# Kernel optimization log

Hardware: AMD Instinct MI355X
Metric: run time of the kernel (lower is better)

The kernel has to match this reference:

```python
import jax, jax.numpy as jnp
import numpy as np

B, T, C, H = 128, 256, 384, 6
D = C // H  # head dim = 64


def setup_inputs() -> dict:
    key = jax.random.key(0)
    k1, k2, k3, k4, k5 = jax.random.split(key, 5)
    s = 0.02
    return {
        "x": jax.random.normal(k1, (B, T, C), dtype=jnp.float32),
        "W_qkv": jax.random.normal(k2, (C, 3 * C), dtype=jnp.float32) * s,
        "b_qkv": jax.random.normal(k3, (3 * C,), dtype=jnp.float32) * s,
        "W_proj": jax.random.normal(k4, (C, C), dtype=jnp.float32) * s,
        "b_proj": jax.random.normal(k5, (C,), dtype=jnp.float32) * s,
    }


def reference(x, W_qkv, b_qkv, W_proj, b_proj):
    Bv, Tv, Cv = x.shape
    # fused QKV projection, then split
    qkv = x @ W_qkv + b_qkv                      # [B,T,3C]
    q, k, v = jnp.split(qkv, 3, axis=-1)
    # [B,T,C] -> [B,H,T,D]
    q = q.reshape(Bv, Tv, H, D).transpose(0, 2, 1, 3)
    k = k.reshape(Bv, Tv, H, D).transpose(0, 2, 1, 3)
    v = v.reshape(Bv, Tv, H, D).transpose(0, 2, 1, 3)
    # causal masked scores, scaled by head_dim**-0.5
    scores = jnp.einsum("bhqd,bhkd->bhqk", q, k) * (D ** -0.5)
    causal = jnp.tril(jnp.ones((Tv, Tv), dtype=bool))
    scores = jnp.where(causal, scores, -jnp.inf)
    wt = jax.nn.softmax(scores, axis=-1)
    # dropout layers are identity in eval mode
    out = jnp.einsum("bhqk,bhkd->bhqd", wt, v)   # [B,H,T,D]
    out = out.transpose(0, 2, 1, 3).reshape(Bv, Tv, Cv)
    return out @ W_proj + b_proj
```

## Files before the change

### kernel.cpp

```cpp
#include <hip/hip_runtime.h>

typedef unsigned short u16;
typedef unsigned int u32;
typedef __attribute__((ext_vector_type(4))) float f32x4;
typedef __attribute__((ext_vector_type(8))) __bf16 bf16x8;
typedef __attribute__((ext_vector_type(2))) __bf16 bf16x2;

#define NEGINF (-1e30f)
#define QSCALE 0.18033688011112042f

__device__ __forceinline__ u16 f32_to_bf16(float f) {
  union { float f; unsigned int u; } v;
  v.f = f;
  unsigned int u = v.u;
  u += 0x7fffu + ((u >> 16) & 1u);
  return (u16)(u >> 16);
}

__device__ __forceinline__ u32 pk_bf16(float a, float b) {
  bf16x2 t;
  t.x = (__bf16)a;
  t.y = (__bf16)b;
  return __builtin_bit_cast(u32, t);
}

__device__ __forceinline__ f32x4 mfma_bf16(bf16x8 a, bf16x8 b, f32x4 c) {
  return __builtin_amdgcn_mfma_f32_16x16x32_bf16(a, b, c, 0, 0, 0);
}

#define GLOAD_LDS16(g, l) __builtin_amdgcn_global_load_lds( \
    (const __attribute__((address_space(1))) unsigned int*)(g), \
    (__attribute__((address_space(3))) unsigned int*)(l), 16, 0, 0)

__global__ void k_cvt_all(const float4* __restrict__ x4, u16* __restrict__ xb,
                          const float* __restrict__ Wqkv, u16* __restrict__ wqkvb,
                          const float* __restrict__ Wproj, u16* __restrict__ wprojb) {
  const int bidx = (int)blockIdx.x;
  if (bidx < 12288) {
    int i = bidx * 256 + threadIdx.x;
    float4 v = x4[i];
    uint2 o;
    o.x = (unsigned int)f32_to_bf16(v.x) | ((unsigned int)f32_to_bf16(v.y) << 16);
    o.y = (unsigned int)f32_to_bf16(v.z) | ((unsigned int)f32_to_bf16(v.w) << 16);
    *(uint2*)(xb + (size_t)i * 4) = o;
  } else if (bidx < 14016) {
    int idx = (bidx - 12288) * 256 + threadIdx.x;
    if (idx < 384 * 1152) {
      int k = idx / 1152, n = idx - k * 1152;
      wqkvb[(size_t)n * 384 + k] = f32_to_bf16(Wqkv[idx]);
    }
  } else {
    int idx = (bidx - 14016) * 256 + threadIdx.x;
    if (idx < 384 * 384) {
      int k = idx / 384, n = idx - k * 384;
      wprojb[(size_t)n * 384 + k] = f32_to_bf16(Wproj[idx]);
    }
  }
}

template <bool SW>
__device__ __forceinline__ void gemm256x64(
    const u16* __restrict__ A, const u16* __restrict__ Bt,
    int mBase, int nBase, u16* lsA, u16* lsB,
    f32x4 acc[4][2], int lane, int wv, int wm, int wn) {
  const int l15 = lane & 15;
  size_t aoff[4];
  u32 aldso[4];
#pragma unroll
  for (int jj = 0; jj < 4; ++jj) {
    int c = wv * 256 + jj * 64 + lane;
    int row = c >> 3;
    int kc = (c & 7) ^ (row & 7);
    aoff[jj] = (size_t)(mBase + row) * 384 + kc * 8;
    aldso[jj] = (u32)(wv * 256 + jj * 64) * 8;
  }
  int cb = wv * 64 + lane;
  int brow = cb >> 3;
  size_t boff = (size_t)(nBase + brow) * 384 + (size_t)(((cb & 7) ^ (brow & 7)) * 8);
  u32 bldso = (u32)(wv * 64) * 8;

#define STAGE_T(kt, buf) do { \
  _Pragma("unroll") \
  for (int jj = 0; jj < 4; ++jj) \
    GLOAD_LDS16(A + aoff[jj] + (kt), lsA + (buf) * 16384 + aldso[jj]); \
  GLOAD_LDS16(Bt + boff + (kt), lsB + (buf) * 4096 + bldso); \
  } while (0)

  STAGE_T(0, 0);
#pragma unroll
  for (int t = 0; t < 6; ++t) {
    const int cur = t & 1;
    if (t < 5) {
      STAGE_T((t + 1) * 64, cur ^ 1);
      asm volatile("s_waitcnt vmcnt(5)" ::: "memory");
    } else {
      asm volatile("s_waitcnt vmcnt(0)" ::: "memory");
    }
    __builtin_amdgcn_s_barrier();
    const char* bA = (const char*)(lsA + cur * 16384);
    const char* bB = (const char*)(lsB + cur * 4096);
#pragma unroll
    for (int ks = 0; ks < 2; ++ks) {
      bf16x8 af[4], bfr[2];
#pragma unroll
      for (int i = 0; i < 4; ++i) {
        int row = wm * 64 + i * 16 + l15;
        af[i] = *(const bf16x8*)(bA + row * 128 + (((ks * 4 + (lane >> 4)) ^ (row & 7)) << 4));
      }
#pragma unroll
      for (int j = 0; j < 2; ++j) {
        int row = wn * 32 + j * 16 + l15;
        bfr[j] = *(const bf16x8*)(bB + row * 128 + (((ks * 4 + (lane >> 4)) ^ (row & 7)) << 4));
      }
#pragma unroll
      for (int i = 0; i < 4; ++i)
#pragma unroll
        for (int j = 0; j < 2; ++j)
          acc[i][j] = SW ? mfma_bf16(bfr[j], af[i], acc[i][j])
                         : mfma_bf16(af[i], bfr[j], acc[i][j]);
    }
    __builtin_amdgcn_s_barrier();
  }
#undef STAGE_T
}

__global__ __launch_bounds__(512, 4) void k_qkv(
    const u16* __restrict__ A, const u16* __restrict__ Bt,
    const float* __restrict__ bias,
    u16* __restrict__ Qb, u16* __restrict__ Kb, u16* __restrict__ Vtb) {
  __shared__ __align__(16) u16 lsA[2 * 16384];
  __shared__ __align__(16) u16 lsB[2 * 4096];
  const int tid = threadIdx.x, lane = tid & 63, wv = tid >> 6;
  const int l15 = lane & 15, g = lane >> 4;
  const int wm = wv >> 1, wn = wv & 1;
  const int bid = (int)blockIdx.x;
  const int wgid = (bid & 7) * 288 + (bid >> 3);
  const int mtile = wgid / 18, ntile = wgid % 18;
  const int mBase = mtile * 256, nBase = ntile * 64;
  const int part = ntile / 6;
  const int hh = ntile % 6;
  char* ot = (char*)lsA;

  f32x4 acc[4][2] = {};
  if (part == 2) {
    gemm256x64<false>(A, Bt, mBase, nBase, lsA, lsB, acc, lane, wv, wm, wn);
#pragma unroll
    for (int j = 0; j < 2; ++j) {
      int drow = wn * 32 + j * 16 + l15;
      float bv = bias[nBase + drow];
#pragma unroll
      for (int i = 0; i < 4; ++i) {
        int t0 = wm * 64 + i * 16 + g * 4;
        uint2 w;
        w.x = pk_bf16(acc[i][j][0] + bv, acc[i][j][1] + bv);
        w.y = pk_bf16(acc[i][j][2] + bv, acc[i][j][3] + bv);
        int byte = (drow * 512 + t0 * 2) ^ ((drow & 7) << 4);
        *(uint2*)(ot + byte) = w;
      }
    }
    asm volatile("s_waitcnt lgkmcnt(0)" ::: "memory");
    __builtin_amdgcn_s_barrier();
    size_t obase = (size_t)(mtile * 6 + hh) * (64 * 256);
#pragma unroll
    for (int p = 0; p < 4; ++p) {
      int idx = p * 512 + tid;
      int row = idx >> 5, c = idx & 31;
      uint4 v = *(const uint4*)(ot + row * 512 + (((c ^ (row & 7)) << 4)));
      *(uint4*)(Vtb + obase + (size_t)row * 256 + c * 8) = v;
    }
  } else {
    gemm256x64<true>(A, Bt, mBase, nBase, lsA, lsB, acc, lane, wv, wm, wn);
    const float scale = (part == 0) ? QSCALE : 1.0f;
    u16* dst = (part == 0) ? Qb : Kb;
#pragma unroll
    for (int j = 0; j < 2; ++j) {
      int dbase = wn * 32 + j * 16 + g * 4;
      float4 bv4 = *(const float4*)(bias + nBase + dbase);
#pragma unroll
      for (int i = 0; i < 4; ++i) {
        int trow = wm * 64 + i * 16 + l15;
        uint2 w;
        w.x = pk_bf16((acc[i][j][0] + bv4.x) * scale, (acc[i][j][1] + bv4.y) * scale);
        w.y = pk_bf16((acc[i][j][2] + bv4.z) * scale, (acc[i][j][3] + bv4.w) * scale);
        int byte = (trow * 128 + dbase * 2) ^ ((trow & 7) << 4);
        *(uint2*)(ot + byte) = w;
      }
    }
    asm volatile("s_waitcnt lgkmcnt(0)" ::: "memory");
    __builtin_amdgcn_s_barrier();
    size_t obase = (size_t)(mtile * 6 + hh) * (256 * 64);
#pragma unroll
    for (int p = 0; p < 4; ++p) {
      int idx = p * 512 + tid;
      int row = idx >> 3, c = idx & 7;
      uint4 v = *(const uint4*)(ot + row * 128 + (((c ^ (row & 7)) << 4)));
      *(uint4*)(dst + obase + (size_t)row * 64 + c * 8) = v;
    }
  }
}

__global__ __launch_bounds__(256, 3) void k_attn(
    const u16* __restrict__ Qb, const u16* __restrict__ Kb,
    const u16* __restrict__ Vtb, u16* __restrict__ Ob) {
  __shared__ __align__(16) u16 lsP[4][32 * 64];
  const int lane = threadIdx.x & 63, wv = threadIdx.x >> 6;
  const int l15 = lane & 15, g = lane >> 4;
  const int bid = (int)blockIdx.x;
  const int id2 = (bid & 7) * 192 + (bid >> 3);
  const int bh = id2 >> 1, grp = id2 & 1;
  const int s = grp ? (5 - wv) : ((wv < 2) ? 7 - wv : 3 - wv);
  const int b = bh / 6, h = bh % 6;
  const u16* Qh = Qb + (size_t)bh * (256 * 64);
  const u16* Kh = Kb + (size_t)bh * (256 * 64);
  const u16* Vh = Vtb + (size_t)bh * (64 * 256);
  const int ktiles = (s >> 1) + 1;
  char* pbuf = (char*)&lsP[wv][0];

  bf16x8 qf[2][2];
#pragma unroll
  for (int ks = 0; ks < 2; ++ks)
#pragma unroll
    for (int iq = 0; iq < 2; ++iq)
      qf[ks][iq] = *(const bf16x8*)(Qh + (size_t)(s * 32 + iq * 16 + l15) * 64 + ks * 32 + g * 8);

  f32x4 o[4][2] = {};
  float rl[2] = {0.f, 0.f};

#pragma unroll 1
  for (int kt = 0; kt < ktiles; ++kt) {
    bf16x8 kf[2][4];
#pragma unroll
    for (int ks = 0; ks < 2; ++ks)
#pragma unroll
      for (int jk = 0; jk < 4; ++jk)
        kf[ks][jk] = *(const bf16x8*)(Kh + (size_t)(kt * 64 + jk * 16 + l15) * 64 + ks * 32 + g * 8);

    f32x4 st[4][2] = {};
    __builtin_amdgcn_s_setprio(1);
#pragma unroll
    for (int ks = 0; ks < 2; ++ks)
#pragma unroll
      for (int jk = 0; jk < 4; ++jk)
#pragma unroll
        for (int iq = 0; iq < 2; ++iq)
          st[jk][iq] = mfma_bf16(kf[ks][jk], qf[ks][iq], st[jk][iq]);
    __builtin_amdgcn_s_setprio(0);

    bf16x8 vf[2][4];
#pragma unroll
    for (int ks = 0; ks < 2; ++ks)
#pragma unroll
      for (int jd = 0; jd < 4; ++jd)
        vf[ks][jd] = *(const bf16x8*)(Vh + (size_t)(jd * 16 + l15) * 256 + kt * 64 + ks * 32 + g * 8);

    if (kt == ktiles - 1) {
#pragma unroll
      for (int jk = 0; jk < 4; ++jk)
#pragma unroll
        for (int iq = 0; iq < 2; ++iq)
#pragma unroll
          for (int r = 0; r < 4; ++r)
            if (kt * 64 + jk * 16 + g * 4 + r > s * 32 + iq * 16 + l15)
              st[jk][iq][r] = NEGINF;
    }

    float rs[2] = {0.f, 0.f};
#pragma unroll
    for (int jk = 0; jk < 4; ++jk)
#pragma unroll
      for (int iq = 0; iq < 2; ++iq) {
        float p0 = __builtin_amdgcn_exp2f(st[jk][iq][0]);
        float p1 = __builtin_amdgcn_exp2f(st[jk][iq][1]);
        float p2 = __builtin_amdgcn_exp2f(st[jk][iq][2]);
        float p3 = __builtin_amdgcn_exp2f(st[jk][iq][3]);
        rs[iq] += (p0 + p1) + (p2 + p3);
        int q = iq * 16 + l15;
        int byte = (q * 128 + (jk * 16 + g * 4) * 2) ^ ((q & 7) << 4);
        uint2 w;
        w.x = pk_bf16(p0, p1);
        w.y = pk_bf16(p2, p3);
        *(uint2*)(pbuf + byte) = w;
      }
#pragma unroll
    for (int iq = 0; iq < 2; ++iq) {
      float v = rs[iq];
      v += __shfl_xor(v, 16);
      v += __shfl_xor(v, 32);
      rl[iq] += v;
    }

#pragma unroll
    for (int ks = 0; ks < 2; ++ks) {
      bf16x8 pf[2];
#pragma unroll
      for (int iq = 0; iq < 2; ++iq) {
        int q = iq * 16 + l15;
        pf[iq] = *(const bf16x8*)(pbuf + ((q * 128 + ks * 64 + g * 16) ^ ((q & 7) << 4)));
      }
      __builtin_amdgcn_s_setprio(1);
#pragma unroll
      for (int jd = 0; jd < 4; ++jd)
#pragma unroll
        for (int iq = 0; iq < 2; ++iq)
          o[jd][iq] = mfma_bf16(vf[ks][jd], pf[iq], o[jd][iq]);
      __builtin_amdgcn_s_setprio(0);
    }
  }

#pragma unroll
  for (int iq = 0; iq < 2; ++iq) {
    float inv = 1.0f / rl[iq];
    int q = iq * 16 + l15;
#pragma unroll
    for (int jd = 0; jd < 4; ++jd) {
      uint2 w;
      w.x = pk_bf16(o[jd][iq][0] * inv, o[jd][iq][1] * inv);
      w.y = pk_bf16(o[jd][iq][2] * inv, o[jd][iq][3] * inv);
      int byte = (q * 128 + jd * 32 + g * 8) ^ ((q & 7) << 4);
      *(uint2*)(pbuf + byte) = w;
    }
  }
  asm volatile("s_waitcnt lgkmcnt(0)" ::: "memory");
#pragma unroll
  for (int rep = 0; rep < 4; ++rep) {
    int row = rep * 8 + (lane >> 3);
    int c = lane & 7;
    uint4 v = *(const uint4*)(pbuf + row * 128 + ((c ^ (row & 7)) * 16));
    int t = s * 32 + row;
    *(uint4*)(Ob + ((size_t)(b * 256 + t)) * 384 + h * 64 + c * 8) = v;
  }
}

__device__ __forceinline__ void gemm128sq(
    const u16* __restrict__ A, const u16* __restrict__ Bt,
    int mBase, int nBase, u16* lsA, u16* lsB,
    f32x4 acc[4][4], int lane, int wv) {
  const int l15 = lane & 15, g = lane >> 4;
  const int wm = wv >> 1, wn = wv & 1;
  size_t aoff[4], boff[4];
  u32 ldso[4];
#pragma unroll
  for (int jj = 0; jj < 4; ++jj) {
    int c = jj * 256 + wv * 64 + lane;
    int row = c >> 3;
    int kc = (c & 7) ^ (row & 7);
    aoff[jj] = (size_t)(mBase + row) * 384 + kc * 8;
    boff[jj] = (size_t)(nBase + row) * 384 + kc * 8;
    ldso[jj] = (u32)c * 8;
  }
#pragma unroll 1
  for (int t = 0; t < 6; ++t) {
#pragma unroll
    for (int jj = 0; jj < 4; ++jj) {
      GLOAD_LDS16(A + aoff[jj] + t * 64, lsA + ldso[jj]);
      GLOAD_LDS16(Bt + boff[jj] + t * 64, lsB + ldso[jj]);
    }
    __syncthreads();
#pragma unroll
    for (int ks = 0; ks < 2; ++ks) {
      bf16x8 af[4], bfr[4];
#pragma unroll
      for (int i = 0; i < 4; ++i) {
        int row = wm * 64 + i * 16 + l15;
        af[i] = *(const bf16x8*)((const char*)lsA + row * 128 + (((ks * 4 + g) ^ (row & 7)) << 4));
      }
#pragma unroll
      for (int j = 0; j < 4; ++j) {
        int row = wn * 64 + j * 16 + l15;
        bfr[j] = *(const bf16x8*)((const char*)lsB + row * 128 + (((ks * 4 + g) ^ (row & 7)) << 4));
      }
      __builtin_amdgcn_s_setprio(1);
#pragma unroll
      for (int i = 0; i < 4; ++i)
#pragma unroll
        for (int j = 0; j < 4; ++j)
          acc[i][j] = mfma_bf16(af[i], bfr[j], acc[i][j]);
      __builtin_amdgcn_s_setprio(0);
    }
    __syncthreads();
  }
}

__global__ __launch_bounds__(256, 3) void k_proj(
    const u16* __restrict__ A, const u16* __restrict__ Bt,
    const float* __restrict__ bias, float* __restrict__ out) {
  __shared__ __align__(16) u16 lsA[8192];
  __shared__ __align__(16) u16 lsB[8192];
  const int tid = threadIdx.x, lane = tid & 63, wv = tid >> 6;
  const int l15 = lane & 15, g = lane >> 4;
  const int wm = wv >> 1, wn = wv & 1;
  const int bid = (int)blockIdx.x;
  const int wgid = (bid & 7) * 96 + (bid >> 3);
  const int mBase = (wgid / 3) * 128, nBase = (wgid % 3) * 128;
  f32x4 acc[4][4] = {};
  gemm128sq(A, Bt, mBase, nBase, lsA, lsB, acc, lane, wv);
#pragma unroll
  for (int j = 0; j < 4; ++j) {
    int col = nBase + wn * 64 + j * 16 + l15;
    float bv = bias[col];
#pragma unroll
    for (int i = 0; i < 4; ++i) {
      int m0 = mBase + wm * 64 + i * 16 + g * 4;
#pragma unroll
      for (int r = 0; r < 4; ++r)
        out[(size_t)(m0 + r) * 384 + col] = acc[i][j][r] + bv;
    }
  }
}

extern "C" void kernel_launch(void* const* d_in, const int* in_sizes, int n_in,
                              void* d_out, int out_size, void* d_ws, size_t ws_size,
                              hipStream_t stream) {
  const float* x     = (const float*)d_in[0];
  const float* Wqkv  = (const float*)d_in[1];
  const float* bqkv  = (const float*)d_in[2];
  const float* Wproj = (const float*)d_in[3];
  const float* bproj = (const float*)d_in[4];
  float* out = (float*)d_out;

  char* ws = (char*)d_ws;
  u16* xb     = (u16*)(ws);
  u16* wqkvb  = (u16*)(ws + 25165824);
  u16* wprojb = (u16*)(ws + 26050560);
  u16* Qb     = (u16*)(ws + 26345472);
  u16* Kb     = (u16*)(ws + 51511296);
  u16* Vtb    = (u16*)(ws + 76677120);
  u16* Ob     = (u16*)(ws + 101842944);

  k_cvt_all<<<14592, 256, 0, stream>>>((const float4*)x, xb, Wqkv, wqkvb, Wproj, wprojb);
  k_qkv<<<2304, 512, 0, stream>>>(xb, wqkvb, bqkv, Qb, Kb, Vtb);
  k_attn<<<1536, 256, 0, stream>>>(Qb, Kb, Vtb, Ob);
  k_proj<<<768, 256, 0, stream>>>(Ob, wprojb, bproj, out);
}
```

Measured before the change: 116.7 us.

## Prefetch next K tile into registers and stage V through LDS asynchronously

The attention loop now software-pipelines its global loads. The next K tile is loaded into registers during the current iteration, and V tiles are copied into per-wave swizzled LDS slices with direct global-to-LDS loads issued one iteration ahead. Manual vmcnt waits order the pipeline. This is meant to hide global-load latency behind the MFMA and softmax work, at the cost of more LDS (which may lower occupancy at 3 blocks per CU), extra registers, and fragile hand-counted waits.

```diff
diff --git a/kernel.cpp b/kernel.cpp
--- a/kernel.cpp
+++ b/kernel.cpp
@@ -202,7 +202,8 @@
 __global__ __launch_bounds__(256, 3) void k_attn(
     const u16* __restrict__ Qb, const u16* __restrict__ Kb,
     const u16* __restrict__ Vtb, u16* __restrict__ Ob) {
-  __shared__ __align__(16) u16 lsP[4][32 * 64];
+  __shared__ __align__(16) u16 lsP[4][2048];
+  __shared__ __align__(16) u16 lsV[4][4096];
   const int lane = threadIdx.x & 63, wv = threadIdx.x >> 6;
   const int l15 = lane & 15, g = lane >> 4;
   const int bid = (int)blockIdx.x;
@@ -215,6 +216,16 @@
   const u16* Vh = Vtb + (size_t)bh * (64 * 256);
   const int ktiles = (s >> 1) + 1;
   char* pbuf = (char*)&lsP[wv][0];
+  u16* vslice = &lsV[wv][0];
+
+#define STAGE_V(kt) do { \
+  _Pragma("unroll") \
+  for (int it = 0; it < 8; ++it) { \
+    int c = it * 64 + lane; \
+    int row = c >> 3; \
+    int kc = (c & 7) ^ (row & 7); \
+    GLOAD_LDS16(Vh + (size_t)row * 256 + (kt) * 64 + kc * 8, vslice + it * 512); \
+  } } while (0)
 
   bf16x8 qf[2][2];
 #pragma unroll
@@ -223,17 +234,21 @@
     for (int iq = 0; iq < 2; ++iq)
       qf[ks][iq] = *(const bf16x8*)(Qh + (size_t)(s * 32 + iq * 16 + l15) * 64 + ks * 32 + g * 8);
 
+  bf16x8 kf[2][4];
+#pragma unroll
+  for (int ks = 0; ks < 2; ++ks)
+#pragma unroll
+    for (int jk = 0; jk < 4; ++jk)
+      kf[ks][jk] = *(const bf16x8*)(Kh + (size_t)(jk * 16 + l15) * 64 + ks * 32 + g * 8);
+  STAGE_V(0);
+
   f32x4 o[4][2] = {};
   float rl[2] = {0.f, 0.f};
 
 #pragma unroll 1
   for (int kt = 0; kt < ktiles; ++kt) {
-    bf16x8 kf[2][4];
-#pragma unroll
-    for (int ks = 0; ks < 2; ++ks)
-#pragma unroll
-      for (int jk = 0; jk < 4; ++jk)
-        kf[ks][jk] = *(const bf16x8*)(Kh + (size_t)(kt * 64 + jk * 16 + l15) * 64 + ks * 32 + g * 8);
+    const bool pre = (kt + 1 < ktiles);
+    asm volatile("s_waitcnt vmcnt(8)" ::: "memory");
 
     f32x4 st[4][2] = {};
     __builtin_amdgcn_s_setprio(1);
@@ -246,12 +261,14 @@
           st[jk][iq] = mfma_bf16(kf[ks][jk], qf[ks][iq], st[jk][iq]);
     __builtin_amdgcn_s_setprio(0);
 
-    bf16x8 vf[2][4];
-#pragma unroll
-    for (int ks = 0; ks < 2; ++ks)
-#pragma unroll
-      for (int jd = 0; jd < 4; ++jd)
-        vf[ks][jd] = *(const bf16x8*)(Vh + (size_t)(jd * 16 + l15) * 256 + kt * 64 + ks * 32 + g * 8);
+    bf16x8 kfn[2][4];
+    if (pre) {
+#pragma unroll
+      for (int ks = 0; ks < 2; ++ks)
+#pragma unroll
+        for (int jk = 0; jk < 4; ++jk)
+          kfn[ks][jk] = *(const bf16x8*)(Kh + (size_t)((kt + 1) * 64 + jk * 16 + l15) * 64 + ks * 32 + g * 8);
+    }
 
     if (kt == ktiles - 1) {
 #pragma unroll
@@ -289,23 +306,45 @@
       rl[iq] += v;
     }
 
+    if (pre) {
+      asm volatile("s_waitcnt vmcnt(8)" ::: "memory");
+    } else {
+      asm volatile("s_waitcnt vmcnt(0)" ::: "memory");
+    }
+
 #pragma unroll
     for (int ks = 0; ks < 2; ++ks) {
-      bf16x8 pf[2];
+      bf16x8 pf[2], vfr[4];
 #pragma unroll
       for (int iq = 0; iq < 2; ++iq) {
         int q = iq * 16 + l15;
         pf[iq] = *(const bf16x8*)(pbuf + ((q * 128 + ks * 64 + g * 16) ^ ((q & 7) << 4)));
       }
+#pragma unroll
+      for (int jd = 0; jd < 4; ++jd) {
+        int d = jd * 16 + l15;
+        vfr[jd] = *(const bf16x8*)((char*)vslice + d * 128 + (((ks * 4 + g) ^ (d & 7)) << 4));
+      }
       __builtin_amdgcn_s_setprio(1);
 #pragma unroll
       for (int jd = 0; jd < 4; ++jd)
 #pragma unroll
         for (int iq = 0; iq < 2; ++iq)
-          o[jd][iq] = mfma_bf16(vf[ks][jd], pf[iq], o[jd][iq]);
+          o[jd][iq] = mfma_bf16(vfr[jd], pf[iq], o[jd][iq]);
       __builtin_amdgcn_s_setprio(0);
     }
-  }
+
+    if (pre) {
+      asm volatile("s_waitcnt lgkmcnt(0)" ::: "memory");
+      STAGE_V(kt + 1);
+#pragma unroll
+      for (int ks = 0; ks < 2; ++ks)
+#pragma unroll
+        for (int jk = 0; jk < 4; ++jk)
+          kf[ks][jk] = kfn[ks][jk];
+    }
+  }
+#undef STAGE_V
 
 #pragma unroll
   for (int iq = 0; iq < 2; ++iq) {
```

New measurement: 123.6 us. 5.9% more time.
